# Kernel optimization log

Measured on AMD Instinct MI355X. Metric: run time of the kernel, lower is better.

## Reference

```python
import jax, jax.numpy as jnp
import numpy as np

B, T, C = 4, 2048, 1024
N_HEAD = 16
HEAD_DIM = C // N_HEAD


def setup_inputs() -> dict:
    key = jax.random.key(0)
    ks = jax.random.split(key, 5)
    bound = 1.0 / np.sqrt(C)
    x = jax.random.normal(ks[0], (B, T, C), dtype=jnp.float32)
    W_attn = jax.random.uniform(ks[1], (C, 3 * C), minval=-bound, maxval=bound, dtype=jnp.float32)
    b_attn = jax.random.uniform(ks[2], (3 * C,), minval=-bound, maxval=bound, dtype=jnp.float32)
    W_proj = jax.random.uniform(ks[3], (C, C), minval=-bound, maxval=bound, dtype=jnp.float32)
    b_proj = jax.random.uniform(ks[4], (C,), minval=-bound, maxval=bound, dtype=jnp.float32)
    return {"x": x, "W_attn": W_attn, "b_attn": b_attn, "W_proj": W_proj, "b_proj": b_proj}


def reference(x, W_attn, b_attn, W_proj, b_proj):
    Bx, Tx, Cx = x.shape
    qkv = x @ W_attn + b_attn                       # [B,T,3C]
    q, k, v = jnp.split(qkv, 3, axis=2)
    # [B,T,C] -> [B,H,T,D]
    q = q.reshape(Bx, Tx, N_HEAD, HEAD_DIM).transpose(0, 2, 1, 3)
    k = k.reshape(Bx, Tx, N_HEAD, HEAD_DIM).transpose(0, 2, 1, 3)
    v = v.reshape(Bx, Tx, N_HEAD, HEAD_DIM).transpose(0, 2, 1, 3)
    scale = 1.0 / np.sqrt(HEAD_DIM).astype(np.float32)
    att = jnp.einsum('bhqd,bhkd->bhqk', q, k) * scale   # [B,H,T,T]
    causal = jnp.tril(jnp.ones((Tx, Tx), dtype=bool))
    att = jnp.where(causal[None, None], att, -jnp.inf)
    att = jax.nn.softmax(att, axis=-1)
    y = jnp.einsum('bhqk,bhkd->bhqd', att, v)           # [B,H,T,D]
    y = y.transpose(0, 2, 1, 3).reshape(Bx, Tx, Cx)
    return y @ W_proj + b_proj
```

## Files before the change

### kernel.cpp

```cpp
#include <hip/hip_runtime.h>

#define Bsz 4
#define Tn 2048
#define Cn 1024
#define Hn 16
#define Dn 64
#define Mn (Bsz * Tn)
#define NQKV (3 * Cn)
#define BH (Bsz * Hn)

typedef short bf16x8_t __attribute__((ext_vector_type(8)));
typedef float f32x4 __attribute__((ext_vector_type(4)));

static __device__ __forceinline__ float exp2_fast(float x) {
    return __builtin_amdgcn_exp2f(x);
}

static __device__ __forceinline__ unsigned short f2bf(float f) {
    union { float f; unsigned int u; } v; v.f = f;
    unsigned int r = v.u + 0x7FFFu + ((v.u >> 16) & 1u);
    return (unsigned short)(r >> 16);
}

static __device__ __forceinline__ unsigned int fbits(float f) {
    union { float f; unsigned int u; } v; v.f = f; return v.u;
}

static __device__ __forceinline__ bf16x8_t ld_frag(const unsigned short* p) {
    bf16x8_t r;
    *reinterpret_cast<float4*>(&r) = *reinterpret_cast<const float4*>(p);
    return r;
}

#define ASYNC_COPY16(gp, lp)                                                         \
    __builtin_amdgcn_global_load_lds((__attribute__((address_space(1))) void*)(gp),  \
                                     (__attribute__((address_space(3))) void*)(lp),  \
                                     16, 0, 0)

__global__ void cast_f32_bf16(const float* __restrict__ src,
                              unsigned short* __restrict__ dst, int n4) {
    int i = blockIdx.x * blockDim.x + threadIdx.x;
    if (i < n4) {
        float4 v = reinterpret_cast<const float4*>(src)[i];
        ushort4 o;
        o.x = f2bf(v.x); o.y = f2bf(v.y); o.z = f2bf(v.z); o.w = f2bf(v.w);
        reinterpret_cast<ushort4*>(dst)[i] = o;
    }
}

__global__ void transpose_cast(const float* __restrict__ src,
                               unsigned short* __restrict__ dst, int R, int Cc) {
    __shared__ float tile[32][33];
    int c0 = blockIdx.x * 32, r0 = blockIdx.y * 32;
    int tx = threadIdx.x & 31, ty = threadIdx.x >> 5;
#pragma unroll
    for (int i = 0; i < 4; i++)
        tile[ty + i * 8][tx] = src[(long)(r0 + ty + i * 8) * Cc + c0 + tx];
    __syncthreads();
#pragma unroll
    for (int i = 0; i < 4; i++)
        dst[(long)(c0 + ty + i * 8) * R + r0 + tx] = f2bf(tile[tx][ty + i * 8]);
}

template <int MODE>
__global__ __launch_bounds__(256) void gemm128(const unsigned short* __restrict__ A,
                                               const unsigned short* __restrict__ Bt,
                                               const float* __restrict__ bias,
                                               float* __restrict__ outF,
                                               unsigned short* __restrict__ Qb,
                                               unsigned short* __restrict__ Kb,
                                               unsigned short* __restrict__ Vt,
                                               int M, int N, int Kd) {
    __shared__ __align__(16) unsigned short As[128 * 32];
    __shared__ __align__(16) unsigned short Bs[128 * 32];
    int n0 = blockIdx.x * 128, m0 = blockIdx.y * 128;
    int tid = threadIdx.x;
    int lane = tid & 63, w = tid >> 6;
    int wm = w >> 1, wn = w & 1;
    int quad = lane >> 4, l15 = lane & 15;
    int r = lane >> 2, c = lane & 3;

    const unsigned short* AgBase = A + (long)(m0 + w * 32 + r) * Kd + c * 8;
    const unsigned short* BgBase = Bt + (long)(n0 + w * 32 + r) * Kd + c * 8;
    unsigned short* ldsA = As + (w * 32) * 32;
    unsigned short* ldsB = Bs + (w * 32) * 32;

    f32x4 acc[4][4] = {};

    for (int kb = 0; kb < Kd; kb += 32) {
        ASYNC_COPY16(AgBase + kb, ldsA);
        ASYNC_COPY16(AgBase + 16 * Kd + kb, ldsA + 512);
        ASYNC_COPY16(BgBase + kb, ldsB);
        ASYNC_COPY16(BgBase + 16 * Kd + kb, ldsB + 512);
        __syncthreads();
        bf16x8_t af[4], bfr[4];
#pragma unroll
        for (int i = 0; i < 4; i++)
            af[i] = ld_frag(&As[(wm * 64 + i * 16 + l15) * 32 + quad * 8]);
#pragma unroll
        for (int j = 0; j < 4; j++)
            bfr[j] = ld_frag(&Bs[(wn * 64 + j * 16 + l15) * 32 + quad * 8]);
#pragma unroll
        for (int i = 0; i < 4; i++)
#pragma unroll
            for (int j = 0; j < 4; j++)
                acc[i][j] = __builtin_amdgcn_mfma_f32_16x16x32_bf16(af[i], bfr[j], acc[i][j], 0, 0, 0);
        __syncthreads();
    }

#pragma unroll
    for (int i = 0; i < 4; i++)
#pragma unroll
        for (int j = 0; j < 4; j++) {
            int col = n0 + wn * 64 + j * 16 + l15;
            float bval = bias[col];
#pragma unroll
            for (int rr = 0; rr < 4; rr++) {
                int row = m0 + wm * 64 + i * 16 + quad * 4 + rr;
                float val = acc[i][j][rr] + bval;
                if (MODE == 0) {
                    outF[(long)row * N + col] = val;
                } else {
                    int seg = col >> 10, within = col & 1023;
                    int h = within >> 6, d = within & 63;
                    int b = row >> 11, t = row & 2047;
                    int bh = b * Hn + h;
                    if (seg == 0) {
                        Qb[((long)bh * Tn + t) * Dn + d] = f2bf(val * 0.18033688f);
                    } else if (seg == 1) {
                        Kb[((long)bh * Tn + t) * Dn + d] = f2bf(val);
                    } else {
                        Vt[((long)bh * Dn + d) * Tn + t] = f2bf(val);
                    }
                }
            }
        }
}

__global__ __launch_bounds__(256) void attn_kernel(const unsigned short* __restrict__ Qb,
                                                   const unsigned short* __restrict__ Kb,
                                                   const unsigned short* __restrict__ Vt,
                                                   unsigned short* __restrict__ Yb) {
    __shared__ __align__(16) unsigned short Ks[64 * 72];
    __shared__ __align__(16) unsigned short Vs[64 * 72];
    __shared__ __align__(16) unsigned short Plds[4][2][16 * 72];
    int tid = threadIdx.x, w = tid >> 6, lane = tid & 63;
    int quad = lane >> 4, l15 = lane & 15;

    int flat = blockIdx.y * 8 + blockIdx.x;
    int xcd = flat & 7, slot = flat >> 3;
    int bh = xcd * 8 + (slot >> 3);
    int qx = slot & 7;
    int b = bh >> 4, h = bh & 15;

    const unsigned short* Qh = Qb + (long)bh * Tn * Dn;
    const unsigned short* Kh = Kb + (long)bh * Tn * Dn;
    const unsigned short* Vh = Vt + (long)bh * Dn * Tn;

    int sr = tid >> 3;
    int sc = (tid & 7) * 8;

#pragma unroll 1
    for (int s = 0; s < 2; s++) {
        int qi = s ? (15 - qx) : qx;
        int q0b = qi * 128;
        int nt = 2 * qi + 2;

        bf16x8_t qf[2][2];
#pragma unroll
        for (int h2 = 0; h2 < 2; h2++) {
            int qrow = q0b + h2 * 64 + w * 16 + l15;
            qf[h2][0] = ld_frag(&Qh[qrow * Dn + quad * 8]);
            qf[h2][1] = ld_frag(&Qh[qrow * Dn + 32 + quad * 8]);
        }

        float m_run[2] = {-1e30f, -1e30f}, l_run[2] = {0.f, 0.f};
        f32x4 Of[2][4] = {};

        float4 kr0 = *reinterpret_cast<const float4*>(&Kh[sr * Dn + sc]);
        float4 kr1 = *reinterpret_cast<const float4*>(&Kh[(32 + sr) * Dn + sc]);
        float4 vr0 = *reinterpret_cast<const float4*>(&Vh[sr * Tn + sc]);
        float4 vr1 = *reinterpret_cast<const float4*>(&Vh[(32 + sr) * Tn + sc]);

#pragma unroll 1
        for (int t = 0; t < nt; t++) {
            int kt0 = t * 64;
            __syncthreads();
            *reinterpret_cast<float4*>(&Ks[sr * 72 + sc]) = kr0;
            *reinterpret_cast<float4*>(&Ks[(32 + sr) * 72 + sc]) = kr1;
            *reinterpret_cast<float4*>(&Vs[sr * 72 + sc]) = vr0;
            *reinterpret_cast<float4*>(&Vs[(32 + sr) * 72 + sc]) = vr1;
            if (t + 1 < nt) {
                int kn = kt0 + 64;
                kr0 = *reinterpret_cast<const float4*>(&Kh[(kn + sr) * Dn + sc]);
                kr1 = *reinterpret_cast<const float4*>(&Kh[(kn + 32 + sr) * Dn + sc]);
                vr0 = *reinterpret_cast<const float4*>(&Vh[sr * Tn + kn + sc]);
                vr1 = *reinterpret_cast<const float4*>(&Vh[(32 + sr) * Tn + kn + sc]);
            }
            __syncthreads();

            bool act0 = (kt0 <= q0b);

            f32x4 st[2][4];
#pragma unroll
            for (int ti = 0; ti < 4; ti++) {
                bf16x8_t ka0 = ld_frag(&Ks[(ti * 16 + l15) * 72 + quad * 8]);
                bf16x8_t ka1 = ld_frag(&Ks[(ti * 16 + l15) * 72 + 32 + quad * 8]);
                if (act0) {
                    f32x4 z = {};
                    z = __builtin_amdgcn_mfma_f32_16x16x32_bf16(ka0, qf[0][0], z, 0, 0, 0);
                    st[0][ti] = __builtin_amdgcn_mfma_f32_16x16x32_bf16(ka1, qf[0][1], z, 0, 0, 0);
                }
                f32x4 z1 = {};
                z1 = __builtin_amdgcn_mfma_f32_16x16x32_bf16(ka0, qf[1][0], z1, 0, 0, 0);
                st[1][ti] = __builtin_amdgcn_mfma_f32_16x16x32_bf16(ka1, qf[1][1], z1, 0, 0, 0);
            }

            bf16x8_t pa[2][2];
#pragma unroll
            for (int h2 = 0; h2 < 2; h2++) {
                int qbase = q0b + h2 * 64;
                if (h2 == 0 && !act0) continue;
                if (kt0 == qbase) {
                    int q_glob = qbase + w * 16 + l15;
#pragma unroll
                    for (int ti = 0; ti < 4; ti++)
#pragma unroll
                        for (int rr = 0; rr < 4; rr++)
                            if (kt0 + ti * 16 + quad * 4 + rr > q_glob) st[h2][ti][rr] = -1e30f;
                }
                float lmax = st[h2][0][0];
#pragma unroll
                for (int ti = 0; ti < 4; ti++)
#pragma unroll
                    for (int rr = 0; rr < 4; rr++) lmax = fmaxf(lmax, st[h2][ti][rr]);
                lmax = fmaxf(lmax, __shfl_xor(lmax, 16));
                lmax = fmaxf(lmax, __shfl_xor(lmax, 32));
                float m_new = fmaxf(m_run[h2], lmax);
                float alpha = exp2_fast(m_run[h2] - m_new);
                float lsum = 0.f;
#pragma unroll
                for (int ti = 0; ti < 4; ti++)
#pragma unroll
                    for (int rr = 0; rr < 4; rr++) {
                        float e = exp2_fast(st[h2][ti][rr] - m_new);
                        st[h2][ti][rr] = e;
                        lsum += e;
                    }
                lsum += __shfl_xor(lsum, 16);
                lsum += __shfl_xor(lsum, 32);
                l_run[h2] = l_run[h2] * alpha + lsum;
                m_run[h2] = m_new;
#pragma unroll
                for (int rr = 0; rr < 4; rr++) {
                    float a_rr = __shfl(alpha, quad * 4 + rr);
#pragma unroll
                    for (int dt = 0; dt < 4; dt++) Of[h2][dt][rr] *= a_rr;
                }
                unsigned short* Pw = &Plds[w][h2][0];
#pragma unroll
                for (int ti = 0; ti < 4; ti++) {
                    unsigned u0 = fbits(st[h2][ti][0]) + 0x8000u;
                    unsigned u1 = fbits(st[h2][ti][1]) + 0x8000u;
                    unsigned u2 = fbits(st[h2][ti][2]) + 0x8000u;
                    unsigned u3 = fbits(st[h2][ti][3]) + 0x8000u;
                    uint2 pk;
                    pk.x = __builtin_amdgcn_perm(u1, u0, 0x07060302);
                    pk.y = __builtin_amdgcn_perm(u3, u2, 0x07060302);
                    *reinterpret_cast<uint2*>(&Pw[l15 * 72 + ti * 16 + quad * 4]) = pk;
                }
#pragma unroll
                for (int kc = 0; kc < 2; kc++)
                    pa[h2][kc] = ld_frag(&Pw[l15 * 72 + kc * 32 + quad * 8]);
            }

#pragma unroll
            for (int kc = 0; kc < 2; kc++)
#pragma unroll
                for (int dt = 0; dt < 4; dt++) {
                    bf16x8_t vb = ld_frag(&Vs[(dt * 16 + l15) * 72 + kc * 32 + quad * 8]);
                    if (act0)
                        Of[0][dt] = __builtin_amdgcn_mfma_f32_16x16x32_bf16(pa[0][kc], vb, Of[0][dt], 0, 0, 0);
                    Of[1][dt] = __builtin_amdgcn_mfma_f32_16x16x32_bf16(pa[1][kc], vb, Of[1][dt], 0, 0, 0);
                }
        }

#pragma unroll
        for (int h2 = 0; h2 < 2; h2++) {
            int qw = q0b + h2 * 64 + w * 16;
#pragma unroll
            for (int rr = 0; rr < 4; rr++) {
                float linv = 1.f / __shfl(l_run[h2], quad * 4 + rr);
                int t = qw + quad * 4 + rr;
                long rowbase = ((long)(b * Tn + t)) * Cn + h * Dn;
#pragma unroll
                for (int dt = 0; dt < 4; dt++)
                    Yb[rowbase + dt * 16 + l15] = f2bf(Of[h2][dt][rr] * linv);
            }
        }
    }
}

extern "C" void kernel_launch(void* const* d_in, const int* in_sizes, int n_in,
                              void* d_out, int out_size, void* d_ws, size_t ws_size,
                              hipStream_t stream) {
    const float* x      = (const float*)d_in[0];
    const float* W_attn = (const float*)d_in[1];
    const float* b_attn = (const float*)d_in[2];
    const float* W_proj = (const float*)d_in[3];
    const float* b_proj = (const float*)d_in[4];
    float* out = (float*)d_out;

    unsigned short* xb      = (unsigned short*)d_ws;
    unsigned short* Wqkv_t  = xb + (size_t)Mn * Cn;
    unsigned short* Wproj_t = Wqkv_t + (size_t)NQKV * Cn;
    unsigned short* Qb      = Wproj_t + (size_t)Cn * Cn;
    unsigned short* Kb      = Qb + (size_t)BH * Tn * Dn;
    unsigned short* Vt      = Kb + (size_t)BH * Tn * Dn;
    unsigned short* Yb      = Vt + (size_t)BH * Tn * Dn;

    cast_f32_bf16<<<(Mn * Cn / 4 + 255) / 256, 256, 0, stream>>>(x, xb, Mn * Cn / 4);
    transpose_cast<<<dim3(NQKV / 32, Cn / 32), 256, 0, stream>>>(W_attn, Wqkv_t, Cn, NQKV);
    transpose_cast<<<dim3(Cn / 32, Cn / 32), 256, 0, stream>>>(W_proj, Wproj_t, Cn, Cn);

    gemm128<1><<<dim3(NQKV / 128, Mn / 128), 256, 0, stream>>>(
        xb, Wqkv_t, b_attn, nullptr, Qb, Kb, Vt, Mn, NQKV, Cn);

    attn_kernel<<<dim3(8, BH), 256, 0, stream>>>(Qb, Kb, Vt, Yb);

    gemm128<0><<<dim3(Cn / 128, Mn / 128), 256, 0, stream>>>(
        Yb, Wproj_t, b_proj, out, nullptr, nullptr, nullptr, Mn, Cn, Cn);
}
```

Before: 309.1 us.

## Replace 128x128 GEMM with double-buffered 256x256 ping-pong MFMA kernel

```diff
diff --git a/kernel.cpp b/kernel.cpp
--- a/kernel.cpp
+++ b/kernel.cpp
@@ -36,6 +36,8 @@
     __builtin_amdgcn_global_load_lds((__attribute__((address_space(1))) void*)(gp),  \
                                      (__attribute__((address_space(3))) void*)(lp),  \
                                      16, 0, 0)
+
+#define MFMA_B16(a, b, c) __builtin_amdgcn_mfma_f32_16x16x32_bf16(a, b, c, 0, 0, 0)
 
 __global__ void cast_f32_bf16(const float* __restrict__ src,
                               unsigned short* __restrict__ dst, int n4) {
@@ -62,75 +64,150 @@
         dst[(long)(c0 + ty + i * 8) * R + r0 + tx] = f2bf(tile[tx][ty + i * 8]);
 }
 
+static __device__ __forceinline__ void stage_tile(const unsigned short* __restrict__ G,
+                                                  int rowBase, int Kd, int kb,
+                                                  unsigned short* lds, int tid) {
+    int r = tid >> 3;
+    int sg = (tid & 7) ^ (r & 7);
+    const unsigned short* gp = G + (long)(rowBase + r) * Kd + kb + sg * 8;
+    unsigned short* lb = lds + (tid >> 6) * 512;
+#pragma unroll
+    for (int l = 0; l < 4; ++l)
+        ASYNC_COPY16(gp + (long)(l * 64) * Kd, lb + l * 4096);
+}
+
+static __device__ __forceinline__ bf16x8_t frag(const unsigned short* lds, int row, int cs) {
+    return ld_frag(lds + row * 64 + ((cs ^ (row & 7)) << 3));
+}
+
 template <int MODE>
-__global__ __launch_bounds__(256) void gemm128(const unsigned short* __restrict__ A,
+__global__ __launch_bounds__(512) void gemm256(const unsigned short* __restrict__ A,
                                                const unsigned short* __restrict__ Bt,
                                                const float* __restrict__ bias,
                                                float* __restrict__ outF,
                                                unsigned short* __restrict__ Qb,
                                                unsigned short* __restrict__ Kb,
                                                unsigned short* __restrict__ Vt,
-                                               int M, int N, int Kd) {
-    __shared__ __align__(16) unsigned short As[128 * 32];
-    __shared__ __align__(16) unsigned short Bs[128 * 32];
-    int n0 = blockIdx.x * 128, m0 = blockIdx.y * 128;
+                                               int M, int N, int Kd, int NBN) {
+    __shared__ __align__(16) unsigned short smem[4 * 16384];
     int tid = threadIdx.x;
     int lane = tid & 63, w = tid >> 6;
-    int wm = w >> 1, wn = w & 1;
+    int wm = w >> 2, wn = w & 3;
     int quad = lane >> 4, l15 = lane & 15;
-    int r = lane >> 2, c = lane & 3;
-
-    const unsigned short* AgBase = A + (long)(m0 + w * 32 + r) * Kd + c * 8;
-    const unsigned short* BgBase = Bt + (long)(n0 + w * 32 + r) * Kd + c * 8;
-    unsigned short* ldsA = As + (w * 32) * 32;
-    unsigned short* ldsB = Bs + (w * 32) * 32;
-
-    f32x4 acc[4][4] = {};
-
-    for (int kb = 0; kb < Kd; kb += 32) {
-        ASYNC_COPY16(AgBase + kb, ldsA);
-        ASYNC_COPY16(AgBase + 16 * Kd + kb, ldsA + 512);
-        ASYNC_COPY16(BgBase + kb, ldsB);
-        ASYNC_COPY16(BgBase + 16 * Kd + kb, ldsB + 512);
-        __syncthreads();
-        bf16x8_t af[4], bfr[4];
-#pragma unroll
-        for (int i = 0; i < 4; i++)
-            af[i] = ld_frag(&As[(wm * 64 + i * 16 + l15) * 32 + quad * 8]);
-#pragma unroll
-        for (int j = 0; j < 4; j++)
-            bfr[j] = ld_frag(&Bs[(wn * 64 + j * 16 + l15) * 32 + quad * 8]);
-#pragma unroll
-        for (int i = 0; i < 4; i++)
-#pragma unroll
-            for (int j = 0; j < 4; j++)
-                acc[i][j] = __builtin_amdgcn_mfma_f32_16x16x32_bf16(af[i], bfr[j], acc[i][j], 0, 0, 0);
-        __syncthreads();
+
+    int nwg = gridDim.x, f = blockIdx.x;
+    int cpx = nwg >> 3;
+    int t = (f & 7) * cpx + (f >> 3);
+    int bm = t / NBN, bn = t - bm * NBN;
+    int m0 = bm << 8, n0 = bn << 8;
+    int NT = Kd >> 6;
+
+    unsigned short* Ab0 = smem;
+    unsigned short* Ab1 = smem + 16384;
+    unsigned short* Bb0 = smem + 32768;
+    unsigned short* Bb1 = smem + 49152;
+
+    stage_tile(A, m0, Kd, 0, Ab0, tid);
+    stage_tile(Bt, n0, Kd, 0, Bb0, tid);
+    stage_tile(A, m0, Kd, 64, Ab1, tid);
+    stage_tile(Bt, n0, Kd, 64, Bb1, tid);
+    asm volatile("s_waitcnt vmcnt(8)" ::: "memory");
+    asm volatile("s_barrier" ::: "memory");
+
+    f32x4 acc[8][4] = {};
+    int arow = wm * 128 + l15;
+    int brow = wn * 64 + l15;
+
+#pragma unroll 1
+    for (int kt = 0; kt < NT; ++kt) {
+        unsigned short* Al = (kt & 1) ? Ab1 : Ab0;
+        unsigned short* Bl = (kt & 1) ? Bb1 : Bb0;
+        bf16x8_t a0k0[4], a1k0[4], a0k1[4], a1k1[4], bk0[4], bk1[4];
+
+#pragma unroll
+        for (int i = 0; i < 4; ++i) a0k0[i] = frag(Al, arow + i * 16, quad);
+#pragma unroll
+        for (int i = 0; i < 4; ++i) a1k0[i] = frag(Al, arow + 64 + i * 16, quad);
+#pragma unroll
+        for (int n = 0; n < 4; ++n) bk0[n] = frag(Bl, brow + n * 16, quad);
+        asm volatile("s_barrier" ::: "memory");
+        asm volatile("s_waitcnt lgkmcnt(0)" ::: "memory");
+        __builtin_amdgcn_s_setprio(1);
+#pragma unroll
+        for (int i = 0; i < 4; ++i)
+#pragma unroll
+            for (int n = 0; n < 4; ++n)
+                acc[i][n] = MFMA_B16(a0k0[i], bk0[n], acc[i][n]);
+        __builtin_amdgcn_s_setprio(0);
+        asm volatile("s_barrier" ::: "memory");
+
+#pragma unroll
+        for (int i = 0; i < 4; ++i) a0k1[i] = frag(Al, arow + i * 16, 4 + quad);
+#pragma unroll
+        for (int i = 0; i < 4; ++i) a1k1[i] = frag(Al, arow + 64 + i * 16, 4 + quad);
+#pragma unroll
+        for (int n = 0; n < 4; ++n) bk1[n] = frag(Bl, brow + n * 16, 4 + quad);
+        asm volatile("s_barrier" ::: "memory");
+        asm volatile("s_waitcnt lgkmcnt(0)" ::: "memory");
+        __builtin_amdgcn_s_setprio(1);
+#pragma unroll
+        for (int i = 0; i < 4; ++i)
+#pragma unroll
+            for (int n = 0; n < 4; ++n)
+                acc[4 + i][n] = MFMA_B16(a1k0[i], bk0[n], acc[4 + i][n]);
+        __builtin_amdgcn_s_setprio(0);
+        asm volatile("s_barrier" ::: "memory");
+
+        if (kt + 2 < NT) stage_tile(A, m0, Kd, (kt + 2) * 64, Al, tid);
+        asm volatile("s_barrier" ::: "memory");
+        __builtin_amdgcn_s_setprio(1);
+#pragma unroll
+        for (int i = 0; i < 4; ++i)
+#pragma unroll
+            for (int n = 0; n < 4; ++n)
+                acc[i][n] = MFMA_B16(a0k1[i], bk1[n], acc[i][n]);
+        __builtin_amdgcn_s_setprio(0);
+        asm volatile("s_barrier" ::: "memory");
+
+        if (kt + 2 < NT) stage_tile(Bt, n0, Kd, (kt + 2) * 64, Bl, tid);
+        asm volatile("s_barrier" ::: "memory");
+        __builtin_amdgcn_s_setprio(1);
+#pragma unroll
+        for (int i = 0; i < 4; ++i)
+#pragma unroll
+            for (int n = 0; n < 4; ++n)
+                acc[4 + i][n] = MFMA_B16(a1k1[i], bk1[n], acc[4 + i][n]);
+        __builtin_amdgcn_s_setprio(0);
+        if (kt + 2 < NT)
+            asm volatile("s_waitcnt vmcnt(8)" ::: "memory");
+        else if (kt + 1 < NT)
+            asm volatile("s_waitcnt vmcnt(0)" ::: "memory");
+        asm volatile("s_barrier" ::: "memory");
     }
 
 #pragma unroll
-    for (int i = 0; i < 4; i++)
-#pragma unroll
-        for (int j = 0; j < 4; j++) {
-            int col = n0 + wn * 64 + j * 16 + l15;
+    for (int mi = 0; mi < 8; ++mi)
+#pragma unroll
+        for (int n = 0; n < 4; ++n) {
+            int col = n0 + wn * 64 + n * 16 + l15;
             float bval = bias[col];
 #pragma unroll
-            for (int rr = 0; rr < 4; rr++) {
-                int row = m0 + wm * 64 + i * 16 + quad * 4 + rr;
-                float val = acc[i][j][rr] + bval;
+            for (int rr = 0; rr < 4; ++rr) {
+                int row = m0 + wm * 128 + mi * 16 + quad * 4 + rr;
+                float val = acc[mi][n][rr] + bval;
                 if (MODE == 0) {
                     outF[(long)row * N + col] = val;
                 } else {
                     int seg = col >> 10, within = col & 1023;
                     int h = within >> 6, d = within & 63;
-                    int b = row >> 11, t = row & 2047;
+                    int b = row >> 11, tt = row & 2047;
                     int bh = b * Hn + h;
                     if (seg == 0) {
-                        Qb[((long)bh * Tn + t) * Dn + d] = f2bf(val * 0.18033688f);
+                        Qb[((long)bh * Tn + tt) * Dn + d] = f2bf(val * 0.18033688f);
                     } else if (seg == 1) {
-                        Kb[((long)bh * Tn + t) * Dn + d] = f2bf(val);
+                        Kb[((long)bh * Tn + tt) * Dn + d] = f2bf(val);
                     } else {
-                        Vt[((long)bh * Dn + d) * Tn + t] = f2bf(val);
+                        Vt[((long)bh * Dn + d) * Tn + tt] = f2bf(val);
                     }
                 }
             }
@@ -323,11 +400,11 @@
     transpose_cast<<<dim3(NQKV / 32, Cn / 32), 256, 0, stream>>>(W_attn, Wqkv_t, Cn, NQKV);
     transpose_cast<<<dim3(Cn / 32, Cn / 32), 256, 0, stream>>>(W_proj, Wproj_t, Cn, Cn);
 
-    gemm128<1><<<dim3(NQKV / 128, Mn / 128), 256, 0, stream>>>(
-        xb, Wqkv_t, b_attn, nullptr, Qb, Kb, Vt, Mn, NQKV, Cn);
+    gemm256<1><<<dim3((NQKV / 256) * (Mn / 256)), 512, 0, stream>>>(
+        xb, Wqkv_t, b_attn, nullptr, Qb, Kb, Vt, Mn, NQKV, Cn, NQKV / 256);
 
     attn_kernel<<<dim3(8, BH), 256, 0, stream>>>(Qb, Kb, Vt, Yb);
 
-    gemm128<0><<<dim3(Cn / 128, Mn / 128), 256, 0, stream>>>(
-        Yb, Wproj_t, b_proj, out, nullptr, nullptr, nullptr, Mn, Cn, Cn);
-}
+    gemm256<0><<<dim3((Cn / 256) * (Mn / 256)), 512, 0, stream>>>(
+        Yb, Wproj_t, b_proj, out, nullptr, nullptr, nullptr, Mn, Cn, Cn, Cn / 256);
+}
```

Measured after the change: 321.8 us. +4.1%, slower.
